# Kernel tuning notes

Hardware: AMD Instinct MI355X
Metric: run time of the kernel (lower is better)

Reference implementation:

```python
import jax, jax.numpy as jnp
import numpy as np

TAU = 0.5

def _projection(z, W1, b1, W2, b2):
    h = jax.nn.elu(z @ W1.T + b1)
    return h @ W2.T + b2

def _normalize(x, eps=1e-12):
    n = jnp.linalg.norm(x, axis=1, keepdims=True)
    return x / jnp.maximum(n, eps)

def setup_inputs() -> dict:
    key = jax.random.key(0)
    k = jax.random.split(key, 6)
    N, D, P = 8192, 256, 256
    s = 1.0 / np.sqrt(D)
    return {
        "z1": jax.random.normal(k[0], (N, D), jnp.float32),
        "z2": jax.random.normal(k[1], (N, D), jnp.float32),
        "W1": jax.random.normal(k[2], (P, D), jnp.float32) * s,
        "b1": jnp.zeros((P,), jnp.float32),
        "W2": jax.random.normal(k[3], (D, P), jnp.float32) * s,
        "b2": jnp.zeros((D,), jnp.float32),
    }

def reference(z1, z2, W1, b1, W2, b2):
    h1 = _projection(z1, W1, b1, W2, b2)
    h2 = _projection(z2, W1, b1, W2, b2)
    n1 = _normalize(h1)
    n2 = _normalize(h2)
    f11 = jnp.exp((n1 @ n1.T) / TAU)  # [N,N]
    f22 = jnp.exp((n2 @ n2.T) / TAU)
    f12 = jnp.exp((n1 @ n2.T) / TAU)
    d12 = jnp.diagonal(f12)
    l1 = -jnp.log(d12 / (f11.sum(1) + f12.sum(1) - jnp.diagonal(f11)))
    # sim(h2,h1) = f12.T: diag same, row-sum = column-sum of f12
    l2 = -jnp.log(d12 / (f22.sum(1) + f12.sum(0) - jnp.diagonal(f22)))
    return (l1 + l2) * 0.5
```

## Files before the change

### kernel.cpp

```cpp
#include <hip/hip_runtime.h>
#include <hip/hip_bf16.h>
#include <hip/hip_fp8.h>
#include <stdint.h>

#define Nn 8192
#define TWO_N 16384
#define INV_TAU 2.0f
#define EXP2_SCALE 2.885390081777927f

typedef unsigned short u16;
typedef unsigned char u8;
typedef __bf16 bf16x8 __attribute__((ext_vector_type(8)));
typedef float f32x4 __attribute__((ext_vector_type(4)));
typedef int i32x8 __attribute__((ext_vector_type(8)));

typedef const __attribute__((address_space(1))) void* gas_ptr;
typedef __attribute__((address_space(3))) void* las_ptr;

__device__ __forceinline__ void async_copy16(const void* g, void* l) {
  __builtin_amdgcn_global_load_lds((gas_ptr)g, (las_ptr)l, 16, 0, 0);
}

__device__ __forceinline__ float hw_exp2(float x) {
  return __builtin_amdgcn_exp2f(x);
}

__global__ __launch_bounds__(256)
void wcvt(const float* __restrict__ W1, const float* __restrict__ W2,
          __bf16* __restrict__ Wb) {
  int i = (blockIdx.x * 256 + threadIdx.x) * 8;
  const float* s = (i < 65536) ? (W1 + i) : (W2 + (i - 65536));
  float4 a0 = *(const float4*)s, a1 = *(const float4*)(s + 4);
  bf16x8 v = {(__bf16)a0.x, (__bf16)a0.y, (__bf16)a0.z, (__bf16)a0.w,
              (__bf16)a1.x, (__bf16)a1.y, (__bf16)a1.z, (__bf16)a1.w};
  *(bf16x8*)&Wb[i] = v;
}

__global__ __launch_bounds__(256)
void mlp_norm(const float* __restrict__ z1, const float* __restrict__ z2,
              const __bf16* __restrict__ Wb, const float* __restrict__ b1,
              const float* __restrict__ b2,
              u8* __restrict__ Mf8, float* __restrict__ snorm,
              float* __restrict__ rsum) {
  __shared__ __bf16 sZ[64 * 64];
  __shared__ __bf16 sW[256 * 64];
  __shared__ __bf16 sH[64 * 256];
  const int bx = blockIdx.x;
  const int i0 = bx * 64;
  const float* Zsrc = (bx < 128) ? (z1 + (size_t)i0 * 256)
                                 : (z2 + (size_t)(i0 - Nn) * 256);
  const int t = threadIdx.x;
  const int lane = t & 63, wave = t >> 6;
  const int wn = wave * 64;
  const int fr = lane >> 4, fc = lane & 15;
  const int sw = fc & 7;

  const __bf16* Wb1 = Wb;
  const __bf16* Wb2 = Wb + 65536;

  if (t < 64) rsum[i0 + t] = 0.f;

  f32x4 acc[4][4];
#pragma unroll
  for (int a = 0; a < 4; a++)
#pragma unroll
    for (int b = 0; b < 4; b++) acc[a][b] = (f32x4){0.f, 0.f, 0.f, 0.f};

  for (int k0 = 0; k0 < 256; k0 += 64) {
    __syncthreads();
#pragma unroll
    for (int it = 0; it < 8; ++it) {
      int c = t + 256 * it;
      int row = c >> 3, g = (c & 7) ^ (row & 7);
      async_copy16(Wb1 + (size_t)row * 256 + k0 + g * 8, (void*)&sW[c * 8]);
    }
#pragma unroll
    for (int it = 0; it < 2; ++it) {
      int c = t + 256 * it;
      int row = c >> 3, g = (c & 7) ^ (row & 7);
      const float* s = Zsrc + (size_t)row * 256 + k0 + g * 8;
      float4 a0 = *(const float4*)s, a1 = *(const float4*)(s + 4);
      bf16x8 v = {(__bf16)a0.x, (__bf16)a0.y, (__bf16)a0.z, (__bf16)a0.w,
                  (__bf16)a1.x, (__bf16)a1.y, (__bf16)a1.z, (__bf16)a1.w};
      *(bf16x8*)&sZ[c * 8] = v;
    }
    __syncthreads();
#pragma unroll
    for (int ks = 0; ks < 2; ++ks) {
      bf16x8 af[4], bfr[4];
#pragma unroll
      for (int mi = 0; mi < 4; mi++)
        af[mi] = *(const bf16x8*)&sZ[(mi * 16 + fc) * 64 + (((ks * 4 + fr) ^ sw) * 8)];
#pragma unroll
      for (int ni = 0; ni < 4; ni++)
        bfr[ni] = *(const bf16x8*)&sW[(wn + ni * 16 + fc) * 64 + (((ks * 4 + fr) ^ sw) * 8)];
#pragma unroll
      for (int mi = 0; mi < 4; mi++)
#pragma unroll
        for (int ni = 0; ni < 4; ni++)
          acc[mi][ni] = __builtin_amdgcn_mfma_f32_16x16x32_bf16(af[mi], bfr[ni], acc[mi][ni], 0, 0, 0);
    }
  }

  {
    float bv[4];
#pragma unroll
    for (int ni = 0; ni < 4; ni++) bv[ni] = b1[wn + ni * 16 + fc];
#pragma unroll
    for (int mi = 0; mi < 4; mi++)
#pragma unroll
      for (int ni = 0; ni < 4; ni++) {
        int col = wn + ni * 16 + fc;
        int gc = col >> 3;
#pragma unroll
        for (int r = 0; r < 4; r++) {
          int row = mi * 16 + fr * 4 + r;
          float v = acc[mi][ni][r] + bv[ni];
          v = v > 0.f ? v : (__expf(v) - 1.f);
          int pos = (gc & 24) | ((gc & 7) ^ (row & 7));
          sH[row * 256 + pos * 8 + (col & 7)] = (__bf16)v;
          acc[mi][ni][r] = 0.f;
        }
      }
  }

  for (int k0 = 0; k0 < 256; k0 += 64) {
    __syncthreads();
#pragma unroll
    for (int it = 0; it < 8; ++it) {
      int c = t + 256 * it;
      int row = c >> 3, g = (c & 7) ^ (row & 7);
      async_copy16(Wb2 + (size_t)row * 256 + k0 + g * 8, (void*)&sW[c * 8]);
    }
    __syncthreads();
    const int kgb = k0 >> 3;
#pragma unroll
    for (int ks = 0; ks < 2; ++ks) {
      bf16x8 af[4], bfr[4];
#pragma unroll
      for (int mi = 0; mi < 4; mi++)
        af[mi] = *(const bf16x8*)&sH[(mi * 16 + fc) * 256 + (kgb + (((ks * 4 + fr) ^ sw))) * 8];
#pragma unroll
      for (int ni = 0; ni < 4; ni++)
        bfr[ni] = *(const bf16x8*)&sW[(wn + ni * 16 + fc) * 64 + (((ks * 4 + fr) ^ sw) * 8)];
#pragma unroll
      for (int mi = 0; mi < 4; mi++)
#pragma unroll
        for (int ni = 0; ni < 4; ni++)
          acc[mi][ni] = __builtin_amdgcn_mfma_f32_16x16x32_bf16(af[mi], bfr[ni], acc[mi][ni], 0, 0, 0);
    }
  }

  float bv[4];
#pragma unroll
  for (int ni = 0; ni < 4; ni++) bv[ni] = b2[wn + ni * 16 + fc];

  __syncthreads();
  float* red = (float*)sZ;
  float* red2 = red + 256;

#pragma unroll
  for (int mi = 0; mi < 4; mi++) {
    float ssq[4] = {0.f, 0.f, 0.f, 0.f};
#pragma unroll
    for (int ni = 0; ni < 4; ni++)
#pragma unroll
      for (int r = 0; r < 4; r++) {
        float v = acc[mi][ni][r] + bv[ni];
        acc[mi][ni][r] = v;
        ssq[r] += v * v;
      }
#pragma unroll
    for (int r = 0; r < 4; r++) {
      float v = ssq[r];
#pragma unroll
      for (int off = 1; off < 16; off <<= 1) v += __shfl_xor(v, off, 16);
      if (fc == 0) red[(mi * 16 + fr * 4 + r) * 4 + wave] = v;
    }
  }
  __syncthreads();

#pragma unroll
  for (int mi = 0; mi < 4; mi++) {
    float ssq2[4] = {0.f, 0.f, 0.f, 0.f};
#pragma unroll
    for (int r = 0; r < 4; r++) {
      int row = mi * 16 + fr * 4 + r;
      float ss = red[row * 4] + red[row * 4 + 1] + red[row * 4 + 2] + red[row * 4 + 3];
      float rn = 1.f / fmaxf(sqrtf(ss), 1e-12f);
#pragma unroll
      for (int ni = 0; ni < 4; ni++) {
        float v = acc[mi][ni][r] * rn;
        __hip_fp8_e4m3 q(v);
        Mf8[(size_t)(i0 + row) * 256 + wn + ni * 16 + fc] = q.__x;
        float fv = (float)q;
        ssq2[r] += fv * fv;
      }
    }
#pragma unroll
    for (int r = 0; r < 4; r++) {
      float v = ssq2[r];
#pragma unroll
      for (int off = 1; off < 16; off <<= 1) v += __shfl_xor(v, off, 16);
      if (fc == 0) red2[(mi * 16 + fr * 4 + r) * 4 + wave] = v;
    }
  }
  __syncthreads();
  if (t < 64)
    snorm[i0 + t] = red2[t * 4] + red2[t * 4 + 1] + red2[t * 4 + 2] + red2[t * 4 + 3];
}

__global__ __launch_bounds__(256, 2)
void gram_sym(const u8* __restrict__ Mf8, float* __restrict__ rsum) {
  __shared__ u8 sB8[2][128 * 256];
  const int t = threadIdx.x;
  const int lane = t & 63, wave = t >> 6;
  const int wm = (wave >> 1) * 64, wn = (wave & 1) * 64;
  const int fr = lane >> 4, fc = lane & 15;

  int f = 2111 - blockIdx.x;
  int b = 0;
  while (f >= 2 * (b + 1) * (b + 2)) ++b;
  int rem = f - 2 * b * (b + 1);
  int r = rem / (b + 1);
  int q = rem - r * (b + 1);
  int k = 4 * b + 1 + r;
  const int i_t = 128 - k;
  const int jt0 = i_t + 4 * q;
  const int L = min(4, k - 4 * q);
  const int i0 = i_t * 128;

  {
    const u8* Bg = Mf8 + (size_t)jt0 * 128 * 256;
#pragma unroll
    for (int it = 0; it < 8; ++it) {
      int c = t + 256 * it;
      int row = c >> 4, slot = c & 15;
      int g = slot ^ (row & 15);
      async_copy16(Bg + (size_t)row * 256 + g * 16, (void*)&sB8[0][c * 16]);
    }
  }

  i32x8 afr[4][2];
  {
    const u8* Ag = Mf8 + (size_t)i0 * 256;
#pragma unroll
    for (int mi = 0; mi < 4; ++mi) {
      const u8* rp = Ag + (size_t)(wm + mi * 16 + fc) * 256 + fr * 32;
#pragma unroll
      for (int kb = 0; kb < 2; ++kb) {
        int4 lo = *(const int4*)(rp + kb * 128);
        int4 hi = *(const int4*)(rp + kb * 128 + 16);
        afr[mi][kb] = (i32x8){lo.x, lo.y, lo.z, lo.w, hi.x, hi.y, hi.z, hi.w};
      }
    }
  }

  float rowacc[4][4];
  float colps[4][4];
#pragma unroll
  for (int a = 0; a < 4; a++)
#pragma unroll
    for (int rr = 0; rr < 4; rr++) { rowacc[a][rr] = 0.f; colps[a][rr] = 0.f; }

#pragma unroll
  for (int jt = 0; jt < 4; ++jt) {
    if (jt < L) {
      const int j_t = jt0 + jt;
      const u8* sB = &sB8[jt & 1][0];

      __syncthreads();

      if (jt + 1 < L) {
        const u8* Bg = Mf8 + (size_t)(j_t + 1) * 128 * 256;
        u8* dst = &sB8[(jt + 1) & 1][0];
#pragma unroll
        for (int it = 0; it < 8; ++it) {
          int c = t + 256 * it;
          int row = c >> 4, slot = c & 15;
          int g = slot ^ (row & 15);
          async_copy16(Bg + (size_t)row * 256 + g * 16, (void*)&dst[c * 16]);
        }
      }

      f32x4 acc[4][4];
#pragma unroll
      for (int a = 0; a < 4; a++)
#pragma unroll
        for (int bb = 0; bb < 4; bb++) acc[a][bb] = (f32x4){0.f, 0.f, 0.f, 0.f};

#pragma unroll
      for (int kb = 0; kb < 2; ++kb) {
        i32x8 bfrag[4];
#pragma unroll
        for (int ni = 0; ni < 4; ++ni) {
          const u8* base = sB + (wn + ni * 16 + fc) * 256;
          int g0 = kb * 8 + fr * 2;
          int4 lo = *(const int4*)(base + ((g0 ^ fc) * 16));
          int4 hi = *(const int4*)(base + (((g0 + 1) ^ fc) * 16));
          bfrag[ni] = (i32x8){lo.x, lo.y, lo.z, lo.w, hi.x, hi.y, hi.z, hi.w};
        }
#pragma unroll
        for (int mi = 0; mi < 4; mi++)
#pragma unroll
          for (int ni = 0; ni < 4; ni++)
            acc[mi][ni] = __builtin_amdgcn_mfma_scale_f32_16x16x128_f8f6f4(
                afr[mi][kb], bfrag[ni], acc[mi][ni], 0, 0, 0, 0x7F, 0, 0x7F);
      }

#pragma unroll
      for (int mi = 0; mi < 4; mi++) {
#pragma unroll
        for (int ni = 0; ni < 4; ni++) {
          float e0 = hw_exp2(acc[mi][ni][0] * EXP2_SCALE);
          float e1 = hw_exp2(acc[mi][ni][1] * EXP2_SCALE);
          float e2 = hw_exp2(acc[mi][ni][2] * EXP2_SCALE);
          float e3 = hw_exp2(acc[mi][ni][3] * EXP2_SCALE);
          rowacc[mi][0] += e0; rowacc[mi][1] += e1;
          rowacc[mi][2] += e2; rowacc[mi][3] += e3;
          colps[jt][ni] += e0 + e1 + e2 + e3;
        }
      }
    }
  }

#pragma unroll
  for (int jt = 0; jt < 4; ++jt) {
    if (jt < L) {
      const int j_t = jt0 + jt;
      if (j_t != i_t) {
        const int j0 = j_t * 128;
#pragma unroll
        for (int ni = 0; ni < 4; ni++) {
          float v = colps[jt][ni];
          v += __shfl_xor(v, 16, 64);
          v += __shfl_xor(v, 32, 64);
          if (fr == 0) atomicAdd(&rsum[j0 + wn + ni * 16 + fc], v);
        }
      }
    }
  }

#pragma unroll
  for (int mi = 0; mi < 4; mi++) {
#pragma unroll
    for (int rr = 0; rr < 4; rr++) {
      float v = rowacc[mi][rr];
#pragma unroll
      for (int off = 1; off < 16; off <<= 1) v += __shfl_xor(v, off, 16);
      rowacc[mi][rr] = v;
    }
  }
  if (fc == 0) {
#pragma unroll
    for (int mi = 0; mi < 4; mi++) {
      int rbase = i0 + wm + mi * 16 + fr * 4;
      atomicAdd(&rsum[rbase + 0], rowacc[mi][0]);
      atomicAdd(&rsum[rbase + 1], rowacc[mi][1]);
      atomicAdd(&rsum[rbase + 2], rowacc[mi][2]);
      atomicAdd(&rsum[rbase + 3], rowacc[mi][3]);
    }
  }
}

__global__ void final_loss(const u8* __restrict__ Mf8, const float* __restrict__ rsum,
                           const float* __restrict__ snorm, float* __restrict__ out) {
  int i = blockIdx.x * 4 + (threadIdx.x >> 6);
  int lane = threadIdx.x & 63;
  unsigned int ua = ((const unsigned int*)(Mf8 + (size_t)i * 256))[lane];
  unsigned int ub = ((const unsigned int*)(Mf8 + (size_t)(Nn + i) * 256))[lane];
  float d = 0.f;
#pragma unroll
  for (int e = 0; e < 4; ++e) {
    __hip_fp8_e4m3 qa, qb;
    qa.__x = (ua >> (8 * e)) & 0xFF;
    qb.__x = (ub >> (8 * e)) & 0xFF;
    d += (float)qa * (float)qb;
  }
#pragma unroll
  for (int off = 32; off; off >>= 1) d += __shfl_xor(d, off, 64);
  if (lane == 0) {
    float den1 = rsum[i] - __expf(snorm[i] * INV_TAU);
    float den2 = rsum[Nn + i] - __expf(snorm[Nn + i] * INV_TAU);
    out[i] = 0.5f * (logf(den1) + logf(den2)) - d * INV_TAU;
  }
}

extern "C" void kernel_launch(void* const* d_in, const int* in_sizes, int n_in,
                              void* d_out, int out_size, void* d_ws, size_t ws_size,
                              hipStream_t stream) {
  const float* z1 = (const float*)d_in[0];
  const float* z2 = (const float*)d_in[1];
  const float* W1 = (const float*)d_in[2];
  const float* b1 = (const float*)d_in[3];
  const float* W2 = (const float*)d_in[4];
  const float* b2 = (const float*)d_in[5];
  float* out = (float*)d_out;

  char* ws = (char*)d_ws;
  u8*     Mf8   = (u8*)(ws);
  float*  rsum  = (float*)(ws + (4u << 20));
  float*  snorm = (float*)(ws + (4u << 20) + 65536);
  __bf16* Wb    = (__bf16*)(ws + (4u << 20) + 131072);

  wcvt<<<64, 256, 0, stream>>>(W1, W2, Wb);

  mlp_norm<<<256, 256, 0, stream>>>(z1, z2, Wb, b1, b2, Mf8, snorm, rsum);

  gram_sym<<<2112, 256, 0, stream>>>(Mf8, rsum);

  final_loss<<<Nn / 4, 256, 0, stream>>>(Mf8, rsum, snorm, out);
}
```

Baseline: 167.4 us.

## Double-buffer MLP weight and input tiles and raise priority around MFMA block

The projection kernel now double-buffers its shared-memory tiles for W1, W2 and z. The next K-slice is prefetched (async global-to-LDS for the weights, register staging for z) while MFMAs run on the current slice, and the first W2 tile is prefetched before the ELU epilogue. This is meant to hide global load latency and drops one barrier per iteration in the second GEMM. The cost is roughly double the LDS use, which may lower occupancy. Separately, the FP8 similarity kernel raises wave priority with s_setprio around its MFMA batch, to favour issuing matrix instructions over competing waves.

```diff
diff --git a/kernel.cpp b/kernel.cpp
--- a/kernel.cpp
+++ b/kernel.cpp
@@ -42,8 +42,8 @@
               const float* __restrict__ b2,
               u8* __restrict__ Mf8, float* __restrict__ snorm,
               float* __restrict__ rsum) {
-  __shared__ __bf16 sZ[64 * 64];
-  __shared__ __bf16 sW[256 * 64];
+  __shared__ __bf16 sZ[2][64 * 64];
+  __shared__ __bf16 sW[2][256 * 64];
   __shared__ __bf16 sH[64 * 256];
   const int bx = blockIdx.x;
   const int i0 = bx * 64;
@@ -58,6 +58,9 @@
   const __bf16* Wb1 = Wb;
   const __bf16* Wb2 = Wb + 65536;
 
+  const int zr0 = t >> 3,         zg0 = (t & 7) ^ (zr0 & 7);
+  const int zr1 = (t + 256) >> 3, zg1 = ((t + 256) & 7) ^ (zr1 & 7);
+
   if (t < 64) rsum[i0 + t] = 0.f;
 
   f32x4 acc[4][4];
@@ -66,40 +69,71 @@
 #pragma unroll
     for (int b = 0; b < 4; b++) acc[a][b] = (f32x4){0.f, 0.f, 0.f, 0.f};
 
-  for (int k0 = 0; k0 < 256; k0 += 64) {
+  float4 za0, za1, zb0, zb1;
+
+#pragma unroll
+  for (int it = 0; it < 8; ++it) {
+    int c = t + 256 * it;
+    int row = c >> 3, g = (c & 7) ^ (row & 7);
+    async_copy16(Wb1 + (size_t)row * 256 + 0 + g * 8, (void*)&sW[0][c * 8]);
+  }
+  {
+    const float* s0 = Zsrc + (size_t)zr0 * 256 + 0 + zg0 * 8;
+    const float* s1 = Zsrc + (size_t)zr1 * 256 + 0 + zg1 * 8;
+    za0 = *(const float4*)s0; za1 = *(const float4*)(s0 + 4);
+    zb0 = *(const float4*)s1; zb1 = *(const float4*)(s1 + 4);
+  }
+
+  for (int idx = 0; idx < 4; ++idx) {
+    const int k0 = idx * 64;
     __syncthreads();
-#pragma unroll
-    for (int it = 0; it < 8; ++it) {
-      int c = t + 256 * it;
-      int row = c >> 3, g = (c & 7) ^ (row & 7);
-      async_copy16(Wb1 + (size_t)row * 256 + k0 + g * 8, (void*)&sW[c * 8]);
-    }
-#pragma unroll
-    for (int it = 0; it < 2; ++it) {
-      int c = t + 256 * it;
-      int row = c >> 3, g = (c & 7) ^ (row & 7);
-      const float* s = Zsrc + (size_t)row * 256 + k0 + g * 8;
-      float4 a0 = *(const float4*)s, a1 = *(const float4*)(s + 4);
-      bf16x8 v = {(__bf16)a0.x, (__bf16)a0.y, (__bf16)a0.z, (__bf16)a0.w,
-                  (__bf16)a1.x, (__bf16)a1.y, (__bf16)a1.z, (__bf16)a1.w};
-      *(bf16x8*)&sZ[c * 8] = v;
+    {
+      bf16x8 v0 = {(__bf16)za0.x, (__bf16)za0.y, (__bf16)za0.z, (__bf16)za0.w,
+                   (__bf16)za1.x, (__bf16)za1.y, (__bf16)za1.z, (__bf16)za1.w};
+      bf16x8 v1 = {(__bf16)zb0.x, (__bf16)zb0.y, (__bf16)zb0.z, (__bf16)zb0.w,
+                   (__bf16)zb1.x, (__bf16)zb1.y, (__bf16)zb1.z, (__bf16)zb1.w};
+      *(bf16x8*)&sZ[idx & 1][t * 8] = v0;
+      *(bf16x8*)&sZ[idx & 1][(t + 256) * 8] = v1;
     }
     __syncthreads();
+    if (idx < 3) {
+      const int kn = k0 + 64;
+#pragma unroll
+      for (int it = 0; it < 8; ++it) {
+        int c = t + 256 * it;
+        int row = c >> 3, g = (c & 7) ^ (row & 7);
+        async_copy16(Wb1 + (size_t)row * 256 + kn + g * 8,
+                     (void*)&sW[(idx + 1) & 1][c * 8]);
+      }
+      const float* s0 = Zsrc + (size_t)zr0 * 256 + kn + zg0 * 8;
+      const float* s1 = Zsrc + (size_t)zr1 * 256 + kn + zg1 * 8;
+      za0 = *(const float4*)s0; za1 = *(const float4*)(s0 + 4);
+      zb0 = *(const float4*)s1; zb1 = *(const float4*)(s1 + 4);
+    }
+    const __bf16* cZ = sZ[idx & 1];
+    const __bf16* cW = sW[idx & 1];
 #pragma unroll
     for (int ks = 0; ks < 2; ++ks) {
       bf16x8 af[4], bfr[4];
 #pragma unroll
       for (int mi = 0; mi < 4; mi++)
-        af[mi] = *(const bf16x8*)&sZ[(mi * 16 + fc) * 64 + (((ks * 4 + fr) ^ sw) * 8)];
+        af[mi] = *(const bf16x8*)&cZ[(mi * 16 + fc) * 64 + (((ks * 4 + fr) ^ sw) * 8)];
 #pragma unroll
       for (int ni = 0; ni < 4; ni++)
-        bfr[ni] = *(const bf16x8*)&sW[(wn + ni * 16 + fc) * 64 + (((ks * 4 + fr) ^ sw) * 8)];
+        bfr[ni] = *(const bf16x8*)&cW[(wn + ni * 16 + fc) * 64 + (((ks * 4 + fr) ^ sw) * 8)];
 #pragma unroll
       for (int mi = 0; mi < 4; mi++)
 #pragma unroll
         for (int ni = 0; ni < 4; ni++)
           acc[mi][ni] = __builtin_amdgcn_mfma_f32_16x16x32_bf16(af[mi], bfr[ni], acc[mi][ni], 0, 0, 0);
     }
+  }
+
+#pragma unroll
+  for (int it = 0; it < 8; ++it) {
+    int c = t + 256 * it;
+    int row = c >> 3, g = (c & 7) ^ (row & 7);
+    async_copy16(Wb2 + (size_t)row * 256 + 0 + g * 8, (void*)&sW[0][c * 8]);
   }
 
   {
@@ -124,16 +158,21 @@
       }
   }
 
-  for (int k0 = 0; k0 < 256; k0 += 64) {
+  for (int idx = 0; idx < 4; ++idx) {
+    const int k0 = idx * 64;
     __syncthreads();
-#pragma unroll
-    for (int it = 0; it < 8; ++it) {
-      int c = t + 256 * it;
-      int row = c >> 3, g = (c & 7) ^ (row & 7);
-      async_copy16(Wb2 + (size_t)row * 256 + k0 + g * 8, (void*)&sW[c * 8]);
-    }
-    __syncthreads();
+    if (idx < 3) {
+      const int kn = k0 + 64;
+#pragma unroll
+      for (int it = 0; it < 8; ++it) {
+        int c = t + 256 * it;
+        int row = c >> 3, g = (c & 7) ^ (row & 7);
+        async_copy16(Wb2 + (size_t)row * 256 + kn + g * 8,
+                     (void*)&sW[(idx + 1) & 1][c * 8]);
+      }
+    }
     const int kgb = k0 >> 3;
+    const __bf16* cW = sW[idx & 1];
 #pragma unroll
     for (int ks = 0; ks < 2; ++ks) {
       bf16x8 af[4], bfr[4];
@@ -142,7 +181,7 @@
         af[mi] = *(const bf16x8*)&sH[(mi * 16 + fc) * 256 + (kgb + (((ks * 4 + fr) ^ sw))) * 8];
 #pragma unroll
       for (int ni = 0; ni < 4; ni++)
-        bfr[ni] = *(const bf16x8*)&sW[(wn + ni * 16 + fc) * 64 + (((ks * 4 + fr) ^ sw) * 8)];
+        bfr[ni] = *(const bf16x8*)&cW[(wn + ni * 16 + fc) * 64 + (((ks * 4 + fr) ^ sw) * 8)];
 #pragma unroll
       for (int mi = 0; mi < 4; mi++)
 #pragma unroll
@@ -156,7 +195,7 @@
   for (int ni = 0; ni < 4; ni++) bv[ni] = b2[wn + ni * 16 + fc];
 
   __syncthreads();
-  float* red = (float*)sZ;
+  float* red = (float*)&sZ[0][0];
   float* red2 = red + 256;
 
 #pragma unroll
@@ -300,12 +339,14 @@
           int4 hi = *(const int4*)(base + (((g0 + 1) ^ fc) * 16));
           bfrag[ni] = (i32x8){lo.x, lo.y, lo.z, lo.w, hi.x, hi.y, hi.z, hi.w};
         }
+        __builtin_amdgcn_s_setprio(1);
 #pragma unroll
         for (int mi = 0; mi < 4; mi++)
 #pragma unroll
           for (int ni = 0; ni < 4; ni++)
             acc[mi][ni] = __builtin_amdgcn_mfma_scale_f32_16x16x128_f8f6f4(
                 afr[mi][kb], bfrag[ni], acc[mi][ni], 0, 0, 0, 0x7F, 0, 0x7F);
+        __builtin_amdgcn_s_setprio(0);
       }
 
 #pragma unroll
```

Result: no change. 169.7 us (+1.3%).

## Fuse all stages into one persistent cooperative kernel with grid syncs

Applied to the files above, without the earlier changes.

Replaces four separate kernel launches (weight convert, MLP+normalize, symmetric Gram, final loss) with a single cooperative kernel of 512 blocks. The stages are separated by grid.sync, and the Gram tiles are processed in a persistent loop. The aim is to remove launch overhead and the tail gaps between kernels. In exchange, the Gram work is now statically strided across blocks, which may load-balance worse than hardware scheduling of 2112 blocks. Shared memory is also sized for the largest stage (72KB), which could limit occupancy to fewer than 2 blocks per CU and make the cooperative launch fail over to the old path.

```diff
diff --git a/kernel.cpp b/kernel.cpp
--- a/kernel.cpp
+++ b/kernel.cpp
@@ -1,7 +1,10 @@
 #include <hip/hip_runtime.h>
+#include <hip/hip_cooperative_groups.h>
 #include <hip/hip_bf16.h>
 #include <hip/hip_fp8.h>
 #include <stdint.h>
+
+namespace cg = cooperative_groups;
 
 #define Nn 8192
 #define TWO_N 16384
@@ -25,27 +28,16 @@
   return __builtin_amdgcn_exp2f(x);
 }
 
-__global__ __launch_bounds__(256)
-void wcvt(const float* __restrict__ W1, const float* __restrict__ W2,
-          __bf16* __restrict__ Wb) {
-  int i = (blockIdx.x * 256 + threadIdx.x) * 8;
-  const float* s = (i < 65536) ? (W1 + i) : (W2 + (i - 65536));
-  float4 a0 = *(const float4*)s, a1 = *(const float4*)(s + 4);
-  bf16x8 v = {(__bf16)a0.x, (__bf16)a0.y, (__bf16)a0.z, (__bf16)a0.w,
-              (__bf16)a1.x, (__bf16)a1.y, (__bf16)a1.z, (__bf16)a1.w};
-  *(bf16x8*)&Wb[i] = v;
-}
-
-__global__ __launch_bounds__(256)
-void mlp_norm(const float* __restrict__ z1, const float* __restrict__ z2,
+
+__device__ __forceinline__
+void mlp_body(int bx, u8* smem,
+              const float* __restrict__ z1, const float* __restrict__ z2,
               const __bf16* __restrict__ Wb, const float* __restrict__ b1,
-              const float* __restrict__ b2,
-              u8* __restrict__ Mf8, float* __restrict__ snorm,
-              float* __restrict__ rsum) {
-  __shared__ __bf16 sZ[64 * 64];
-  __shared__ __bf16 sW[256 * 64];
-  __shared__ __bf16 sH[64 * 256];
-  const int bx = blockIdx.x;
+              const float* __restrict__ b2, u8* __restrict__ Mf8,
+              float* __restrict__ snorm, float* __restrict__ rsum) {
+  __bf16* sZ = (__bf16*)(smem);
+  __bf16* sW = (__bf16*)(smem + 8192);
+  __bf16* sH = (__bf16*)(smem + 40960);
   const int i0 = bx * 64;
   const float* Zsrc = (bx < 128) ? (z1 + (size_t)i0 * 256)
                                  : (z2 + (size_t)(i0 - Nn) * 256);
@@ -210,15 +202,17 @@
     snorm[i0 + t] = red2[t * 4] + red2[t * 4 + 1] + red2[t * 4 + 2] + red2[t * 4 + 3];
 }
 
-__global__ __launch_bounds__(256, 2)
-void gram_sym(const u8* __restrict__ Mf8, float* __restrict__ rsum) {
-  __shared__ u8 sB8[2][128 * 256];
+__device__ __forceinline__
+void gram_body(int s, u8* smem, const u8* __restrict__ Mf8,
+               float* __restrict__ rsum) {
+  u8* sB0 = smem;
+  u8* sB1 = smem + 32768;
   const int t = threadIdx.x;
   const int lane = t & 63, wave = t >> 6;
   const int wm = (wave >> 1) * 64, wn = (wave & 1) * 64;
   const int fr = lane >> 4, fc = lane & 15;
 
-  int f = 2111 - blockIdx.x;
+  int f = 2111 - s;
   int b = 0;
   while (f >= 2 * (b + 1) * (b + 2)) ++b;
   int rem = f - 2 * b * (b + 1);
@@ -230,6 +224,8 @@
   const int L = min(4, k - 4 * q);
   const int i0 = i_t * 128;
 
+  __syncthreads();
+
   {
     const u8* Bg = Mf8 + (size_t)jt0 * 128 * 256;
 #pragma unroll
@@ -237,7 +233,7 @@
       int c = t + 256 * it;
       int row = c >> 4, slot = c & 15;
       int g = slot ^ (row & 15);
-      async_copy16(Bg + (size_t)row * 256 + g * 16, (void*)&sB8[0][c * 16]);
+      async_copy16(Bg + (size_t)row * 256 + g * 16, (void*)&sB0[c * 16]);
     }
   }
 
@@ -267,13 +263,13 @@
   for (int jt = 0; jt < 4; ++jt) {
     if (jt < L) {
       const int j_t = jt0 + jt;
-      const u8* sB = &sB8[jt & 1][0];
+      const u8* sB = (jt & 1) ? sB1 : sB0;
 
       __syncthreads();
 
       if (jt + 1 < L) {
         const u8* Bg = Mf8 + (size_t)(j_t + 1) * 128 * 256;
-        u8* dst = &sB8[(jt + 1) & 1][0];
+        u8* dst = ((jt + 1) & 1) ? sB1 : sB0;
 #pragma unroll
         for (int it = 0; it < 8; ++it) {
           int c = t + 256 * it;
@@ -363,10 +359,10 @@
   }
 }
 
-__global__ void final_loss(const u8* __restrict__ Mf8, const float* __restrict__ rsum,
-                           const float* __restrict__ snorm, float* __restrict__ out) {
-  int i = blockIdx.x * 4 + (threadIdx.x >> 6);
-  int lane = threadIdx.x & 63;
+__device__ __forceinline__
+void final_body(int i, int lane, const u8* __restrict__ Mf8,
+                const float* __restrict__ rsum, const float* __restrict__ snorm,
+                float* __restrict__ out) {
   unsigned int ua = ((const unsigned int*)(Mf8 + (size_t)i * 256))[lane];
   unsigned int ub = ((const unsigned int*)(Mf8 + (size_t)(Nn + i) * 256))[lane];
   float d = 0.f;
@@ -384,6 +380,71 @@
     float den2 = rsum[Nn + i] - __expf(snorm[Nn + i] * INV_TAU);
     out[i] = 0.5f * (logf(den1) + logf(den2)) - d * INV_TAU;
   }
+}
+
+__global__ __launch_bounds__(256, 2)
+void fused_all(const float* __restrict__ z1, const float* __restrict__ z2,
+               const float* __restrict__ W1, const float* __restrict__ b1,
+               const float* __restrict__ W2, const float* __restrict__ b2,
+               u8* __restrict__ Mf8, float* __restrict__ rsum,
+               float* __restrict__ snorm, __bf16* __restrict__ Wb,
+               float* __restrict__ out) {
+  __shared__ __align__(16) u8 smem[73728];
+  cg::grid_group grid = cg::this_grid();
+
+  {
+    int gi = blockIdx.x * 256 + threadIdx.x;
+    float v = (gi < 65536) ? W1[gi] : W2[gi - 65536];
+    Wb[gi] = (__bf16)v;
+  }
+  grid.sync();
+
+  if (blockIdx.x < 256)
+    mlp_body(blockIdx.x, smem, z1, z2, Wb, b1, b2, Mf8, snorm, rsum);
+  grid.sync();
+
+  for (int s = blockIdx.x; s < 2112; s += 512)
+    gram_body(s, smem, Mf8, rsum);
+  grid.sync();
+
+  {
+    int wave = threadIdx.x >> 6, lane = threadIdx.x & 63;
+#pragma unroll
+    for (int rr = 0; rr < 4; ++rr)
+      final_body(blockIdx.x * 16 + wave * 4 + rr, lane, Mf8, rsum, snorm, out);
+  }
+}
+
+__global__ __launch_bounds__(256)
+void wcvt(const float* __restrict__ W1, const float* __restrict__ W2,
+          __bf16* __restrict__ Wb) {
+  int i = (blockIdx.x * 256 + threadIdx.x) * 8;
+  const float* s = (i < 65536) ? (W1 + i) : (W2 + (i - 65536));
+  float4 a0 = *(const float4*)s, a1 = *(const float4*)(s + 4);
+  bf16x8 v = {(__bf16)a0.x, (__bf16)a0.y, (__bf16)a0.z, (__bf16)a0.w,
+              (__bf16)a1.x, (__bf16)a1.y, (__bf16)a1.z, (__bf16)a1.w};
+  *(bf16x8*)&Wb[i] = v;
+}
+
+__global__ __launch_bounds__(256)
+void mlp_norm(const float* __restrict__ z1, const float* __restrict__ z2,
+              const __bf16* __restrict__ Wb, const float* __restrict__ b1,
+              const float* __restrict__ b2, u8* __restrict__ Mf8,
+              float* __restrict__ snorm, float* __restrict__ rsum) {
+  __shared__ __align__(16) u8 smem[73728];
+  mlp_body(blockIdx.x, smem, z1, z2, Wb, b1, b2, Mf8, snorm, rsum);
+}
+
+__global__ __launch_bounds__(256, 2)
+void gram_sym(const u8* __restrict__ Mf8, float* __restrict__ rsum) {
+  __shared__ __align__(16) u8 smem[65536];
+  gram_body(blockIdx.x, smem, Mf8, rsum);
+}
+
+__global__ void final_loss(const u8* __restrict__ Mf8, const float* __restrict__ rsum,
+                           const float* __restrict__ snorm, float* __restrict__ out) {
+  int i = blockIdx.x * 4 + (threadIdx.x >> 6);
+  final_body(i, threadIdx.x & 63, Mf8, rsum, snorm, out);
 }
 
 extern "C" void kernel_launch(void* const* d_in, const int* in_sizes, int n_in,
@@ -403,11 +464,16 @@
   float*  snorm = (float*)(ws + (4u << 20) + 65536);
   __bf16* Wb    = (__bf16*)(ws + (4u << 20) + 131072);
 
-  wcvt<<<64, 256, 0, stream>>>(W1, W2, Wb);
-
-  mlp_norm<<<256, 256, 0, stream>>>(z1, z2, Wb, b1, b2, Mf8, snorm, rsum);
-
-  gram_sym<<<2112, 256, 0, stream>>>(Mf8, rsum);
-
-  final_loss<<<Nn / 4, 256, 0, stream>>>(Mf8, rsum, snorm, out);
-}
+  void* args[] = {(void*)&z1, (void*)&z2, (void*)&W1, (void*)&b1,
+                  (void*)&W2, (void*)&b2, (void*)&Mf8, (void*)&rsum,
+                  (void*)&snorm, (void*)&Wb, (void*)&out};
+  hipError_t err = hipLaunchCooperativeKernel((const void*)fused_all,
+                                              dim3(512), dim3(256),
+                                              args, 0, stream);
+  if (err != hipSuccess) {
+    wcvt<<<64, 256, 0, stream>>>(W1, W2, Wb);
+    mlp_norm<<<256, 256, 0, stream>>>(z1, z2, Wb, b1, b2, Mf8, snorm, rsum);
+    gram_sym<<<2112, 256, 0, stream>>>(Mf8, rsum);
+    final_loss<<<Nn / 4, 256, 0, stream>>>(Mf8, rsum, snorm, out);
+  }
+}
```

New measurement: 325.3 us. 94.3% more time.
